# Kernel tuning notes

Hardware: AMD Instinct MI355X
Metric: run time of the kernel (lower is better)

## Reference

```python
import jax, jax.numpy as jnp
import numpy as np

H = 16          # num heads
HD = 88         # head dim = 1408 / 16
IMG = 336
PATCH = 14
THETA = 10000.0
IDX = IMG // PATCH          # 24 patches per side
SEQ = IDX * IDX + 1         # 576 patches + 1 CLS slot = 577


def _vision_rope_cos_sin():
    # Faithful to HF Llama4VisionRotaryEmbedding (rope_type='llama4', complex64):
    # 2D rope over (x, y) patch coordinates; CLS token gets zero rotation.
    img_idx = np.arange(IDX * IDX, dtype=np.int64).reshape(-1, 1)
    img_idx = np.concatenate([img_idx, img_idx[:1]], axis=0)
    img_idx[-1, -1] = -2  # CLS token marker
    fx = img_idx % IDX
    fy = img_idx // IDX
    freq_dim = HD // 2  # 44
    rope_freq = 1.0 / (THETA ** (np.arange(0, freq_dim, 2)[: freq_dim // 2].astype(np.float64) / freq_dim))
    freqs_x = np.repeat((fx + 1)[..., None] * rope_freq[None, None, :], 2, axis=-1)
    freqs_y = np.repeat((fy + 1)[..., None] * rope_freq[None, None, :], 2, axis=-1)
    freqs = np.concatenate([freqs_x, freqs_y], axis=-1)[..., ::2]  # [SEQ, 1, HD//2]
    freqs = np.where(img_idx.reshape(-1, 1, 1) < 0, 0.0, freqs)
    return jnp.asarray(np.cos(freqs), jnp.float32), jnp.asarray(np.sin(freqs), jnp.float32)


def _apply_rope(x, cos, sin):
    # x: [B, S, H, HD]; treat last dim as HD//2 complex pairs, rotate by e^{i*freq}
    xr = x.reshape(*x.shape[:-1], HD // 2, 2)
    a, b = xr[..., 0], xr[..., 1]               # [B, S, H, HD//2]
    out_r = a * cos - b * sin                   # cos/sin [S,1,HD//2] broadcast over B,H
    out_i = a * sin + b * cos
    return jnp.stack([out_r, out_i], axis=-1).reshape(x.shape)


def setup_inputs() -> dict:
    key = jax.random.key(0)
    ks = jax.random.split(key, 9)
    D = H * HD  # 1408
    B, S = 32, SEQ
    s = 0.02
    return {
        "hidden_states": jax.random.normal(ks[0], (B, S, D), jnp.float32),
        "wq": jax.random.normal(ks[1], (D, D), jnp.float32) * s,
        "bq": jax.random.normal(ks[2], (D,), jnp.float32) * s,
        "wk": jax.random.normal(ks[3], (D, D), jnp.float32) * s,
        "bk": jax.random.normal(ks[4], (D,), jnp.float32) * s,
        "wv": jax.random.normal(ks[5], (D, D), jnp.float32) * s,
        "bv": jax.random.normal(ks[6], (D,), jnp.float32) * s,
        "wo": jax.random.normal(ks[7], (D, D), jnp.float32) * s,
        "bo": jax.random.normal(ks[8], (D,), jnp.float32) * s,
    }


def reference(hidden_states, wq, bq, wk, bk, wv, bv, wo, bo):
    B, S, D = hidden_states.shape
    cos, sin = _vision_rope_cos_sin()
    # QKV projections (torch Linear convention: y = x @ W.T + b)
    q = (hidden_states @ wq.T + bq).reshape(B, S, H, HD)
    k = (hidden_states @ wk.T + bk).reshape(B, S, H, HD)
    v = (hidden_states @ wv.T + bv).reshape(B, S, H, HD)
    q = _apply_rope(q, cos, sin)
    k = _apply_rope(k, cos, sin)
    # Full (non-causal) self-attention
    scores = jnp.einsum('bqhd,bkhd->bhqk', q, k) * (HD ** -0.5)
    probs = jax.nn.softmax(scores, axis=-1)
    attn = jnp.einsum('bhqk,bkhd->bqhd', probs, v).reshape(B, S, D)
    return attn @ wo.T + bo
```

## Files before the change

### kernel.cpp

```cpp
#include <hip/hip_runtime.h>
#include <hip/hip_bf16.h>
#include <cstdint>
#include <cstddef>

#define NHEADS 16
#define HDIM   88
#define SEQLEN 577
#define NBATCH 32
#define DMODEL 1408
#define MROWS  (NBATCH * SEQLEN)
#define MTILES 145
#define MPAD   (MTILES * 128)
#define SP     592
#define DP     96
#define SPAD   592
#define NFREQ  44
#define NBH    (NBATCH * NHEADS)
#define PADELEMS 6056

typedef __attribute__((ext_vector_type(8))) short short8;
typedef __attribute__((ext_vector_type(4))) short short4v;
typedef __attribute__((ext_vector_type(4))) float floatx4;

__device__ __forceinline__ unsigned short f2bf(float f) {
    union { float f; unsigned u; } v; v.f = f;
    unsigned u = v.u;
    u += 0x7fffu + ((u >> 16) & 1u);
    return (unsigned short)(u >> 16);
}

__device__ __forceinline__ void gload_lds16(const void* g, void* lds) {
    __builtin_amdgcn_global_load_lds(
        (__attribute__((address_space(1))) unsigned int*)(void*)(g ? (void*)g : (void*)g),
        (__attribute__((address_space(3))) unsigned int*)lds, 16, 0, 0);
}

__global__ void l4v_rope_table(float* __restrict__ cos_t, float* __restrict__ sin_t) {
    int idx = blockIdx.x * blockDim.x + threadIdx.x;
    if (idx >= SEQLEN * NFREQ) return;
    int s = idx / NFREQ, j = idx % NFREQ;
    float ang = 0.0f;
    if (s != SEQLEN - 1) {
        int coord = (j < 22) ? (s % 24) : (s / 24);
        int i = (j < 22) ? j : j - 22;
        float rf = __expf(-(2.0f * (float)i / 44.0f) * 9.21034037197618f);
        ang = (float)(coord + 1) * rf;
    }
    cos_t[idx] = cosf(ang);
    sin_t[idx] = sinf(ang);
}

__global__ void l4v_cvt_bf16(const float* __restrict__ in, unsigned short* __restrict__ out, int n) {
    int i = (blockIdx.x * blockDim.x + threadIdx.x) * 4;
    if (i + 3 < n) {
        float4 f = *(const float4*)(in + i);
        ushort4 o;
        o.x = f2bf(f.x); o.y = f2bf(f.y); o.z = f2bf(f.z); o.w = f2bf(f.w);
        *(ushort4*)(out + i) = o;
    } else {
        for (; i < n; i++) out[i] = f2bf(in[i]);
    }
}

__global__ void l4v_padzero(unsigned short* __restrict__ qb,
                            unsigned short* __restrict__ kb,
                            unsigned short* __restrict__ vb) {
    int idx = blockIdx.x * blockDim.x + threadIdx.x;
    if (idx >= NBH * PADELEMS) return;
    int bh = idx / PADELEMS, r = idx % PADELEMS;
    size_t off;
    if (r < 15 * 96) {
        int row = SEQLEN + r / 96, col = r % 96;
        off = ((size_t)bh * SP + row) * DP + col;
    } else {
        int rr = r - 15 * 96;
        int row = rr / 8, col = 88 + (rr % 8);
        off = ((size_t)bh * SP + row) * DP + col;
    }
    qb[off] = 0; kb[off] = 0; vb[off] = 0;
}

__global__ __launch_bounds__(256)
void l4v_vtr(const unsigned short* __restrict__ vb, unsigned short* __restrict__ vt) {
    __shared__ __align__(16) unsigned short t_sm[16 * 104];
    const int tid = threadIdx.x;
    const int bh  = blockIdx.y;
    const int s0  = blockIdx.x * 16;
    const size_t ibase = (size_t)bh * SP * DP;
    const size_t obase = (size_t)bh * DP * SPAD;
    if (tid < 192) {
        int row = tid / 12, ch = tid % 12;
        short8 v = *(const short8*)(vb + ibase + (size_t)(s0 + row) * DP + ch * 8);
        *(short8*)(t_sm + row * 104 + ch * 8) = v;
    }
    __syncthreads();
    if (tid < 192) {
        int d = tid >> 1, sc = tid & 1;
        short8 o;
#pragma unroll
        for (int j = 0; j < 8; j++) o[j] = (short)t_sm[(sc * 8 + j) * 104 + d];
        *(short8*)(vt + obase + (size_t)d * SPAD + s0 + sc * 8) = o;
    }
}

__global__ __launch_bounds__(256, 2)
void l4v_gemm128(const unsigned short* __restrict__ A,
                 const unsigned short* __restrict__ Bw,
                 const float* __restrict__ bias,
                 const float* __restrict__ cos_t,
                 const float* __restrict__ sin_t,
                 unsigned short* __restrict__ out_bf,
                 float* __restrict__ out_f32,
                 int mode)
{
    __shared__ __align__(16) unsigned short a_sm[128 * 32];
    __shared__ __align__(16) unsigned short b_sm[128 * 32];

    const int tid  = threadIdx.x;
    const int lane = tid & 63;
    const int w    = tid >> 6;
    const int quad = lane >> 4;
    const int c    = lane & 15;
    const int wr   = w >> 1;
    const int wc   = w & 1;
    const int m0   = blockIdx.y * 128;
    const int n0   = blockIdx.x * 128;

    floatx4 acc[4][4];
#pragma unroll
    for (int i = 0; i < 4; i++)
#pragma unroll
        for (int j = 0; j < 4; j++) acc[i][j] = (floatx4)0.0f;

    const int chunk0 = w * 128 + lane;
    const int chunk1 = w * 128 + 64 + lane;
    const int r0 = chunk0 >> 2, ch0 = chunk0 & 3;
    const int r1 = chunk1 >> 2, ch1 = chunk1 & 3;
    const unsigned short* Ab = A  + (size_t)m0 * DMODEL;
    const unsigned short* Bb = Bw + (size_t)n0 * DMODEL;

    for (int k0 = 0; k0 < DMODEL; k0 += 32) {
        gload_lds16(Ab + (size_t)r0 * DMODEL + k0 + ch0 * 8, a_sm + (w * 128) * 8);
        gload_lds16(Ab + (size_t)r1 * DMODEL + k0 + ch1 * 8, a_sm + (w * 128 + 64) * 8);
        gload_lds16(Bb + (size_t)r0 * DMODEL + k0 + ch0 * 8, b_sm + (w * 128) * 8);
        gload_lds16(Bb + (size_t)r1 * DMODEL + k0 + ch1 * 8, b_sm + (w * 128 + 64) * 8);
        __syncthreads();
        short8 af[4], bfr[4];
#pragma unroll
        for (int mt = 0; mt < 4; mt++)
            af[mt] = *(const short8*)(a_sm + (wr * 64 + mt * 16 + c) * 32 + quad * 8);
#pragma unroll
        for (int nt = 0; nt < 4; nt++)
            bfr[nt] = *(const short8*)(b_sm + (wc * 64 + nt * 16 + c) * 32 + quad * 8);
#pragma unroll
        for (int mt = 0; mt < 4; mt++)
#pragma unroll
            for (int nt = 0; nt < 4; nt++)
                acc[mt][nt] = __builtin_amdgcn_mfma_f32_16x16x32_bf16(af[mt], bfr[nt], acc[mt][nt], 0, 0, 0);
        __syncthreads();
    }

    if (mode == 3) {
#pragma unroll
        for (int mt = 0; mt < 4; mt++) {
            int mbase = m0 + wr * 64 + mt * 16 + quad * 4;
#pragma unroll
            for (int nt = 0; nt < 4; nt++) {
                int n = n0 + wc * 64 + nt * 16 + c;
                float bi = bias[n];
#pragma unroll
                for (int r = 0; r < 4; r++) {
                    int m = mbase + r;
                    if (m < MROWS) out_f32[(size_t)m * DMODEL + n] = acc[mt][nt][r] + bi;
                }
            }
        }
        return;
    }

    const bool rope = (mode < 2);
#pragma unroll
    for (int mt = 0; mt < 4; mt++) {
        int mbase = m0 + wr * 64 + mt * 16 + quad * 4;
#pragma unroll
        for (int nt = 0; nt < 4; nt++) {
            int n = n0 + wc * 64 + nt * 16 + c;
            float bi = bias[n];
            int h = n / HDIM, d = n % HDIM, j = d >> 1;
#pragma unroll
            for (int r = 0; r < 4; r++) {
                int m = mbase + r;
                int s = m % SEQLEN;
                int b = m / SEQLEN;
                float v = acc[mt][nt][r] + bi;
                float outv = v;
                if (rope) {
                    float pv = __shfl_xor(v, 1);
                    float cs = cos_t[s * NFREQ + j];
                    float sn = sin_t[s * NFREQ + j];
                    outv = ((d & 1) == 0) ? (v * cs - pv * sn) : (pv * sn + v * cs);
                }
                if (m < MROWS)
                    out_bf[((size_t)(b * NHEADS + h) * SP + s) * DP + d] = f2bf(outv);
            }
        }
    }
}

__global__ __launch_bounds__(256, 2)
void l4v_attn(const unsigned short* __restrict__ Q,
              const unsigned short* __restrict__ K,
              const unsigned short* __restrict__ Vt,
              unsigned short* __restrict__ Obuf)
{
    __shared__ __align__(16) unsigned short k_sm[64 * 104];
    __shared__ __align__(16) unsigned short v_sm[96 * 72];
    __shared__ __align__(16) unsigned short p_sm[4][16 * 68];

    const int tid  = threadIdx.x;
    const int lane = tid & 63;
    const int w    = tid >> 6;
    const int quad = lane >> 4;
    const int c    = lane & 15;
    const int qt   = blockIdx.x;
    const int bh   = blockIdx.y;
    const size_t base = (size_t)bh * SP * DP;
    const size_t vtb  = (size_t)bh * DP * SPAD;

    short8 aq[3];
    {
        int qrow = qt * 64 + w * 16 + c;
        if (qrow > SP - 1) qrow = SP - 1;
#pragma unroll
        for (int ks = 0; ks < 3; ks++)
            aq[ks] = *(const short8*)(Q + base + (size_t)qrow * DP + ks * 32 + quad * 8);
    }

    float m_run[4], l_run[4];
    floatx4 o_acc[6];
#pragma unroll
    for (int r = 0; r < 4; r++) { m_run[r] = -INFINITY; l_run[r] = 0.0f; }
#pragma unroll
    for (int i = 0; i < 6; i++) o_acc[i] = (floatx4)0.0f;

    const float sl2e = 0.10660035817780522f * 1.4426950408889634f;

    for (int kt = 0; kt < 10; kt++) {
#pragma unroll
        for (int i = 0; i < 4; i++) {
            int chnk = i * 256 + tid;
            if (chnk < 64 * 13) {
                int row = chnk / 13, pos = chnk - row * 13;
                int gpos = (pos < 12) ? pos : 0;
                int krow = kt * 64 + row;
                if (krow > SP - 1) krow = SP - 1;
                gload_lds16(K + base + (size_t)krow * DP + gpos * 8, k_sm + chnk * 8);
            }
        }
#pragma unroll
        for (int i = 0; i < 4; i++) {
            int chnk = i * 256 + tid;
            if (chnk < 96 * 9) {
                int row = chnk / 9, pos = chnk - row * 9;
                int col = kt * 64 + (pos & 7) * 8;
                if (col > 584) col = 584;
                gload_lds16(Vt + vtb + (size_t)row * SPAD + col, v_sm + chnk * 8);
            }
        }
        __syncthreads();

        floatx4 sc[4];
#pragma unroll
        for (int nt = 0; nt < 4; nt++) {
            sc[nt] = (floatx4)0.0f;
#pragma unroll
            for (int ks = 0; ks < 3; ks++) {
                short8 bk = *(const short8*)(k_sm + (nt * 16 + c) * 104 + ks * 32 + quad * 8);
                sc[nt] = __builtin_amdgcn_mfma_f32_16x16x32_bf16(aq[ks], bk, sc[nt], 0, 0, 0);
            }
        }

        float t[4][4];
#pragma unroll
        for (int nt = 0; nt < 4; nt++) {
            int skcol = kt * 64 + nt * 16 + c;
            bool valid = (skcol < SEQLEN);
#pragma unroll
            for (int r = 0; r < 4; r++)
                t[nt][r] = valid ? sc[nt][r] * sl2e : -INFINITY;
        }

        float mnew[4], alpha[4];
#pragma unroll
        for (int r = 0; r < 4; r++) {
            float v = fmaxf(fmaxf(t[0][r], t[1][r]), fmaxf(t[2][r], t[3][r]));
#pragma unroll
            for (int off = 1; off < 16; off <<= 1) v = fmaxf(v, __shfl_xor(v, off));
            mnew[r] = fmaxf(m_run[r], v);
            alpha[r] = exp2f(m_run[r] - mnew[r]);
            m_run[r] = mnew[r];
        }

        float p[4][4];
#pragma unroll
        for (int nt = 0; nt < 4; nt++)
#pragma unroll
            for (int r = 0; r < 4; r++)
                p[nt][r] = exp2f(t[nt][r] - mnew[r]);

#pragma unroll
        for (int r = 0; r < 4; r++) {
            float sm = p[0][r] + p[1][r] + p[2][r] + p[3][r];
#pragma unroll
            for (int off = 1; off < 16; off <<= 1) sm += __shfl_xor(sm, off);
            l_run[r] = l_run[r] * alpha[r] + sm;
        }

#pragma unroll
        for (int nt = 0; nt < 4; nt++)
#pragma unroll
            for (int r = 0; r < 4; r++)
                p_sm[w][(quad * 4 + r) * 68 + nt * 16 + c] = f2bf(p[nt][r]);

#pragma unroll
        for (int i = 0; i < 6; i++)
#pragma unroll
            for (int r = 0; r < 4; r++)
                o_acc[i][r] *= alpha[r];

#pragma unroll
        for (int kp = 0; kp < 2; kp++) {
            short8 ap;
            {
                short4v lo = *(const short4v*)(&p_sm[w][c * 68 + kp * 32 + quad * 8]);
                short4v hi = *(const short4v*)(&p_sm[w][c * 68 + kp * 32 + quad * 8 + 4]);
#pragma unroll
                for (int t4 = 0; t4 < 4; t4++) { ap[t4] = lo[t4]; ap[t4 + 4] = hi[t4]; }
            }
#pragma unroll
            for (int d2 = 0; d2 < 6; d2++) {
                short8 bv = *(const short8*)(v_sm + (d2 * 16 + c) * 72 + (kp * 4 + quad) * 8);
                o_acc[d2] = __builtin_amdgcn_mfma_f32_16x16x32_bf16(ap, bv, o_acc[d2], 0, 0, 0);
            }
        }
        __syncthreads();
    }

    const int b = bh >> 4, h = bh & 15;
#pragma unroll
    for (int r = 0; r < 4; r++) {
        int sq = qt * 64 + w * 16 + quad * 4 + r;
        float il = 1.0f / l_run[r];
        if (sq < SEQLEN) {
            size_t rowoff = ((size_t)b * SEQLEN + sq) * DMODEL + h * HDIM;
#pragma unroll
            for (int d2 = 0; d2 < 6; d2++) {
                int d = d2 * 16 + c;
                if (d < HDIM) Obuf[rowoff + d] = f2bf(o_acc[d2][r] * il);
            }
        }
    }
}

extern "C" void kernel_launch(void* const* d_in, const int* in_sizes, int n_in,
                              void* d_out, int out_size, void* d_ws, size_t ws_size,
                              hipStream_t stream)
{
    const float* hs = (const float*)d_in[0];
    const float* wq = (const float*)d_in[1];
    const float* bq = (const float*)d_in[2];
    const float* wk = (const float*)d_in[3];
    const float* bk = (const float*)d_in[4];
    const float* wv = (const float*)d_in[5];
    const float* bv = (const float*)d_in[6];
    const float* wo = (const float*)d_in[7];
    const float* bo = (const float*)d_in[8];
    float* out = (float*)d_out;

    char* ws = (char*)d_ws;
    size_t off = 0;
    auto alloc = [&](size_t bytes) -> char* {
        char* p = ws + off;
        off += (bytes + 255) & ~(size_t)255;
        return p;
    };

    unsigned short* hs_bf = (unsigned short*)alloc((size_t)MPAD * DMODEL * 2);
    unsigned short* wq_bf = (unsigned short*)alloc((size_t)DMODEL * DMODEL * 2);
    unsigned short* wk_bf = (unsigned short*)alloc((size_t)DMODEL * DMODEL * 2);
    unsigned short* wv_bf = (unsigned short*)alloc((size_t)DMODEL * DMODEL * 2);
    unsigned short* wo_bf = (unsigned short*)alloc((size_t)DMODEL * DMODEL * 2);
    unsigned short* qb    = (unsigned short*)alloc((size_t)NBH * SP * DP * 2);
    unsigned short* kb    = (unsigned short*)alloc((size_t)NBH * SP * DP * 2);
    unsigned short* vbuf  = (unsigned short*)alloc((size_t)NBH * SP * DP * 2);
    float* cos_t = (float*)alloc((size_t)SEQLEN * NFREQ * 4);
    float* sin_t = (float*)alloc((size_t)SEQLEN * NFREQ * 4);
    unsigned short* attn_bf = hs_bf;
    unsigned short* vt = (unsigned short*)out;

    if (off > ws_size) return;

    l4v_rope_table<<<dim3((SEQLEN * NFREQ + 255) / 256), dim3(256), 0, stream>>>(cos_t, sin_t);
    l4v_padzero<<<dim3((NBH * PADELEMS + 255) / 256), dim3(256), 0, stream>>>(qb, kb, vbuf);

    const int nhs = MROWS * DMODEL;
    l4v_cvt_bf16<<<dim3(nhs / 4 / 256), dim3(256), 0, stream>>>(hs, hs_bf, nhs);
    const int nw = DMODEL * DMODEL;
    l4v_cvt_bf16<<<dim3(nw / 4 / 256), dim3(256), 0, stream>>>(wq, wq_bf, nw);
    l4v_cvt_bf16<<<dim3(nw / 4 / 256), dim3(256), 0, stream>>>(wk, wk_bf, nw);
    l4v_cvt_bf16<<<dim3(nw / 4 / 256), dim3(256), 0, stream>>>(wv, wv_bf, nw);
    l4v_cvt_bf16<<<dim3(nw / 4 / 256), dim3(256), 0, stream>>>(wo, wo_bf, nw);

    dim3 ggrid(DMODEL / 128, MTILES);
    l4v_gemm128<<<ggrid, dim3(256), 0, stream>>>(hs_bf, wq_bf, bq, cos_t, sin_t, qb, nullptr, 0);
    l4v_gemm128<<<ggrid, dim3(256), 0, stream>>>(hs_bf, wk_bf, bk, cos_t, sin_t, kb, nullptr, 1);
    l4v_gemm128<<<ggrid, dim3(256), 0, stream>>>(hs_bf, wv_bf, bv, cos_t, sin_t, vbuf, nullptr, 2);

    l4v_vtr<<<dim3(37, NBH), dim3(256), 0, stream>>>(vbuf, vt);

    l4v_attn<<<dim3(10, NBH), dim3(256), 0, stream>>>(qb, kb, vt, attn_bf);

    l4v_gemm128<<<ggrid, dim3(256), 0, stream>>>(attn_bf, wo_bf, bo, cos_t, sin_t, nullptr, out, 3);
}
```

Baseline: 1.014 ms.

## Widen GEMM tiles to 128x256 with XCD-aware block mapping and retile V transpose

The projection GEMM now computes 128x256 output tiles, with 8 accumulator fragments per wave, from a flattened 1D grid. Block IDs are remapped so that consecutive tiles land on the same XCD, which is meant to improve L2 reuse of A and B. The V transpose kernel now handles 64 sequence rows per block, with an XOR-swizzled LDS layout to cut bank conflicts. Because 1408 is not a multiple of 256, the last column tile wastes compute. Its B loads also read past the end of the weight rows; the results are discarded, but the reads touch adjacent memory.

```diff
diff --git a/kernel.cpp b/kernel.cpp
--- a/kernel.cpp
+++ b/kernel.cpp
@@ -17,6 +17,8 @@
 #define NFREQ  44
 #define NBH    (NBATCH * NHEADS)
 #define PADELEMS 6056
+#define NT256  6
+#define NWG    (MTILES * NT256)
 
 typedef __attribute__((ext_vector_type(8))) short short8;
 typedef __attribute__((ext_vector_type(4))) short short4v;
@@ -82,29 +84,38 @@
 
 __global__ __launch_bounds__(256)
 void l4v_vtr(const unsigned short* __restrict__ vb, unsigned short* __restrict__ vt) {
-    __shared__ __align__(16) unsigned short t_sm[16 * 104];
+    __shared__ __align__(16) unsigned short t_sm[64 * 128];
     const int tid = threadIdx.x;
     const int bh  = blockIdx.y;
-    const int s0  = blockIdx.x * 16;
+    const int s0  = blockIdx.x * 64;
     const size_t ibase = (size_t)bh * SP * DP;
     const size_t obase = (size_t)bh * DP * SPAD;
-    if (tid < 192) {
-        int row = tid / 12, ch = tid % 12;
-        short8 v = *(const short8*)(vb + ibase + (size_t)(s0 + row) * DP + ch * 8);
-        *(short8*)(t_sm + row * 104 + ch * 8) = v;
+#pragma unroll
+    for (int i = 0; i < 3; i++) {
+        int idx = i * 256 + tid;
+        int row = idx / 12, ch = idx - row * 12;
+        int srow = s0 + row; if (srow > SP - 1) srow = SP - 1;
+        short8 v = *(const short8*)(vb + ibase + (size_t)srow * DP + ch * 8);
+        *(short8*)(t_sm + row * 128 + ((ch ^ (row >> 3)) << 3)) = v;
     }
     __syncthreads();
-    if (tid < 192) {
-        int d = tid >> 1, sc = tid & 1;
+#pragma unroll
+    for (int i = 0; i < 3; i++) {
+        int idx = i * 256 + tid;
+        int d = idx >> 3, sc = idx & 7;
+        int cb = d >> 3, dl = d & 7;
         short8 o;
 #pragma unroll
-        for (int j = 0; j < 8; j++) o[j] = (short)t_sm[(sc * 8 + j) * 104 + d];
-        *(short8*)(vt + obase + (size_t)d * SPAD + s0 + sc * 8) = o;
+        for (int j = 0; j < 8; j++)
+            o[j] = (short)t_sm[(sc * 8 + j) * 128 + ((cb ^ sc) << 3) + dl];
+        int s = s0 + sc * 8;
+        if (s <= SPAD - 8)
+            *(short8*)(vt + obase + (size_t)d * SPAD + s) = o;
     }
 }
 
 __global__ __launch_bounds__(256, 2)
-void l4v_gemm128(const unsigned short* __restrict__ A,
+void l4v_gemm256(const unsigned short* __restrict__ A,
                  const unsigned short* __restrict__ Bw,
                  const float* __restrict__ bias,
                  const float* __restrict__ cos_t,
@@ -114,7 +125,7 @@
                  int mode)
 {
     __shared__ __align__(16) unsigned short a_sm[128 * 32];
-    __shared__ __align__(16) unsigned short b_sm[128 * 32];
+    __shared__ __align__(16) unsigned short b_sm[256 * 32];
 
     const int tid  = threadIdx.x;
     const int lane = tid & 63;
@@ -123,39 +134,51 @@
     const int c    = lane & 15;
     const int wr   = w >> 1;
     const int wc   = w & 1;
-    const int m0   = blockIdx.y * 128;
-    const int n0   = blockIdx.x * 128;
-
-    floatx4 acc[4][4];
+
+    const int bid = blockIdx.x;
+    const int xcd = bid & 7, idx = bid >> 3;
+    const int wg  = (xcd < 6) ? xcd * 109 + idx : 6 * 109 + (xcd - 6) * 108 + idx;
+    const int m0  = (wg / NT256) * 128;
+    const int n0  = (wg % NT256) * 256;
+
+    floatx4 acc[4][8];
 #pragma unroll
     for (int i = 0; i < 4; i++)
 #pragma unroll
-        for (int j = 0; j < 4; j++) acc[i][j] = (floatx4)0.0f;
+        for (int j = 0; j < 8; j++) acc[i][j] = (floatx4)0.0f;
 
     const int chunk0 = w * 128 + lane;
     const int chunk1 = w * 128 + 64 + lane;
     const int r0 = chunk0 >> 2, ch0 = chunk0 & 3;
     const int r1 = chunk1 >> 2, ch1 = chunk1 & 3;
+    int rb[4], cbp[4];
+#pragma unroll
+    for (int j = 0; j < 4; j++) {
+        int chnk = j * 256 + tid;
+        rb[j] = chnk >> 2; cbp[j] = chnk & 3;
+    }
     const unsigned short* Ab = A  + (size_t)m0 * DMODEL;
     const unsigned short* Bb = Bw + (size_t)n0 * DMODEL;
 
     for (int k0 = 0; k0 < DMODEL; k0 += 32) {
         gload_lds16(Ab + (size_t)r0 * DMODEL + k0 + ch0 * 8, a_sm + (w * 128) * 8);
         gload_lds16(Ab + (size_t)r1 * DMODEL + k0 + ch1 * 8, a_sm + (w * 128 + 64) * 8);
-        gload_lds16(Bb + (size_t)r0 * DMODEL + k0 + ch0 * 8, b_sm + (w * 128) * 8);
-        gload_lds16(Bb + (size_t)r1 * DMODEL + k0 + ch1 * 8, b_sm + (w * 128 + 64) * 8);
+#pragma unroll
+        for (int j = 0; j < 4; j++)
+            gload_lds16(Bb + (size_t)rb[j] * DMODEL + k0 + cbp[j] * 8,
+                        b_sm + (j * 256 + w * 64) * 8);
         __syncthreads();
-        short8 af[4], bfr[4];
+        short8 af[4], bfr[8];
 #pragma unroll
         for (int mt = 0; mt < 4; mt++)
             af[mt] = *(const short8*)(a_sm + (wr * 64 + mt * 16 + c) * 32 + quad * 8);
 #pragma unroll
-        for (int nt = 0; nt < 4; nt++)
-            bfr[nt] = *(const short8*)(b_sm + (wc * 64 + nt * 16 + c) * 32 + quad * 8);
+        for (int nt = 0; nt < 8; nt++)
+            bfr[nt] = *(const short8*)(b_sm + (wc * 128 + nt * 16 + c) * 32 + quad * 8);
 #pragma unroll
         for (int mt = 0; mt < 4; mt++)
 #pragma unroll
-            for (int nt = 0; nt < 4; nt++)
+            for (int nt = 0; nt < 8; nt++)
                 acc[mt][nt] = __builtin_amdgcn_mfma_f32_16x16x32_bf16(af[mt], bfr[nt], acc[mt][nt], 0, 0, 0);
         __syncthreads();
     }
@@ -165,8 +188,9 @@
         for (int mt = 0; mt < 4; mt++) {
             int mbase = m0 + wr * 64 + mt * 16 + quad * 4;
 #pragma unroll
-            for (int nt = 0; nt < 4; nt++) {
-                int n = n0 + wc * 64 + nt * 16 + c;
+            for (int nt = 0; nt < 8; nt++) {
+                int n = n0 + wc * 128 + nt * 16 + c;
+                if (n >= DMODEL) continue;
                 float bi = bias[n];
 #pragma unroll
                 for (int r = 0; r < 4; r++) {
@@ -183,8 +207,9 @@
     for (int mt = 0; mt < 4; mt++) {
         int mbase = m0 + wr * 64 + mt * 16 + quad * 4;
 #pragma unroll
-        for (int nt = 0; nt < 4; nt++) {
-            int n = n0 + wc * 64 + nt * 16 + c;
+        for (int nt = 0; nt < 8; nt++) {
+            int n = n0 + wc * 128 + nt * 16 + c;
+            if (n >= DMODEL) continue;
             float bi = bias[n];
             int h = n / HDIM, d = n % HDIM, j = d >> 1;
 #pragma unroll
@@ -411,14 +436,13 @@
     l4v_cvt_bf16<<<dim3(nw / 4 / 256), dim3(256), 0, stream>>>(wv, wv_bf, nw);
     l4v_cvt_bf16<<<dim3(nw / 4 / 256), dim3(256), 0, stream>>>(wo, wo_bf, nw);
 
-    dim3 ggrid(DMODEL / 128, MTILES);
-    l4v_gemm128<<<ggrid, dim3(256), 0, stream>>>(hs_bf, wq_bf, bq, cos_t, sin_t, qb, nullptr, 0);
-    l4v_gemm128<<<ggrid, dim3(256), 0, stream>>>(hs_bf, wk_bf, bk, cos_t, sin_t, kb, nullptr, 1);
-    l4v_gemm128<<<ggrid, dim3(256), 0, stream>>>(hs_bf, wv_bf, bv, cos_t, sin_t, vbuf, nullptr, 2);
-
-    l4v_vtr<<<dim3(37, NBH), dim3(256), 0, stream>>>(vbuf, vt);
+    l4v_gemm256<<<dim3(NWG), dim3(256), 0, stream>>>(hs_bf, wq_bf, bq, cos_t, sin_t, qb, nullptr, 0);
+    l4v_gemm256<<<dim3(NWG), dim3(256), 0, stream>>>(hs_bf, wk_bf, bk, cos_t, sin_t, kb, nullptr, 1);
+    l4v_gemm256<<<dim3(NWG), dim3(256), 0, stream>>>(hs_bf, wv_bf, bv, cos_t, sin_t, vbuf, nullptr, 2);
+
+    l4v_vtr<<<dim3(10, NBH), dim3(256), 0, stream>>>(vbuf, vt);
 
     l4v_attn<<<dim3(10, NBH), dim3(256), 0, stream>>>(qb, kb, vt, attn_bf);
 
-    l4v_gemm128<<<ggrid, dim3(256), 0, stream>>>(attn_bf, wo_bf, bo, cos_t, sin_t, nullptr, out, 3);
-}
+    l4v_gemm256<<<dim3(NWG), dim3(256), 0, stream>>>(attn_bf, wo_bf, bo, cos_t, sin_t, nullptr, out, 3);
+}
```

After: 1.045 ms. 3.0% more time.
